# Kernel optimization log

Hardware: AMD Instinct MI355X
Metric: run time of the kernel (lower is better)

Reference implementation:

```python
import jax, jax.numpy as jnp
import numpy as np

B, N, M, C, H = 2, 2048, 512, 1536, 12
HD = C // H          # 128 head dim
RD = 64              # partial rotary dim (rotary_dim in torch code)
EPS = 1e-6


def setup_inputs() -> dict:
    key = jax.random.key(0)
    ks = jax.random.split(key, 8)
    x = jax.random.normal(ks[0], (B, N, C), dtype=jnp.float32)
    y = jax.random.normal(ks[1], (B, M, C), dtype=jnp.float32)
    # realistic rope table: pos[n, j, 0]=cos, pos[n, j, 1]=sin, j over RD//2 freqs
    t = jnp.arange(N, dtype=jnp.float32)
    inv_freq = 1.0 / (10000.0 ** (jnp.arange(RD // 2, dtype=jnp.float32) / (RD // 2)))
    ang = t[:, None] * inv_freq[None, :]                     # [N, RD/2]
    pos = jnp.stack([jnp.cos(ang), jnp.sin(ang)], axis=-1)   # [N, RD/2, 2]
    y_token_weights = jax.random.uniform(ks[2], (B, M), dtype=jnp.float32, minval=0.05, maxval=2.0)
    s = 0.02
    Wqkv = jax.random.normal(ks[3], (C, 3 * C), dtype=jnp.float32) * s
    Wkv = jax.random.normal(ks[4], (C, 2 * C), dtype=jnp.float32) * s
    q_norm_w = jnp.ones((HD,), dtype=jnp.float32)
    k_norm_w = jnp.ones((HD,), dtype=jnp.float32)
    Wproj = jax.random.normal(ks[5], (C, C), dtype=jnp.float32) * s
    bproj = jnp.zeros((C,), dtype=jnp.float32)
    return {"x": x, "y": y, "pos": pos, "y_token_weights": y_token_weights,
            "Wqkv": Wqkv, "Wkv": Wkv, "q_norm_w": q_norm_w, "k_norm_w": k_norm_w,
            "Wproj": Wproj, "bproj": bproj}


def _rms_norm(h, w):
    # RMSNorm in fp32 then cast back (matches torch Norm)
    hf = h.astype(jnp.float32)
    var = jnp.mean(hf * hf, axis=-1, keepdims=True)
    return (w * (hf * jax.lax.rsqrt(var + EPS))).astype(h.dtype)


def _rope(q, k, pos):
    # q,k: [B,H,N,HD]; pos: [N, RD/2, 2]; rotate first RD dims only
    cos = pos[..., 0][None, None]            # [1,1,N,RD/2]
    sin = pos[..., 1][None, None]
    half = RD // 2

    def rot(t):
        t1 = t[..., :half]
        t2 = t[..., half:RD]
        t_rot = jnp.concatenate([t1 * cos - t2 * sin, t1 * sin + t2 * cos], axis=-1)
        return jnp.concatenate([t_rot, t[..., RD:]], axis=-1)

    return rot(q), rot(k)


def reference(x, y, pos, y_token_weights, Wqkv, Wkv, q_norm_w, k_norm_w, Wproj, bproj):
    # self QKV: [B,N,3C] -> [3,B,H,N,HD]
    qkv = jnp.einsum('bnc,cd->bnd', x, Wqkv).reshape(B, N, 3, H, HD).transpose(2, 0, 3, 1, 4)
    q, kx, vx = qkv[0], qkv[1], qkv[2]
    q = _rms_norm(q, q_norm_w)
    kx = _rms_norm(kx, k_norm_w)
    q, kx = _rope(q, kx, pos)

    # cross KV from y: [B,M,2C] -> [2,B,H,M,HD]
    kv = jnp.einsum('bmc,cd->bmd', y, Wkv).reshape(B, M, 2, H, HD).transpose(2, 0, 3, 1, 4)
    ky = _rms_norm(kv[0], k_norm_w)
    vy = kv[1]
    k = jnp.concatenate([kx, ky], axis=2)    # [B,H,N+M,HD]
    v = jnp.concatenate([vx, vy], axis=2)

    # additive bias: zeros over x tokens, log(clamp(w)) over y tokens
    y_bias = jnp.log(jnp.clip(y_token_weights, 1e-4, None))           # [B,M]
    attn_bias = jnp.concatenate([jnp.zeros((B, N), x.dtype), y_bias], axis=1)[:, None, None, :]

    scale = HD ** -0.5
    scores = jnp.einsum('bhnd,bhsd->bhns', q, k) * scale + attn_bias  # [B,H,N,N+M]
    attn = jax.nn.softmax(scores, axis=-1)
    out = jnp.einsum('bhns,bhsd->bhnd', attn, v)                      # [B,H,N,HD]
    out = out.transpose(0, 2, 1, 3).reshape(B, N, C)
    return jnp.einsum('bnc,cd->bnd', out, Wproj) + bproj
```

## Files before the change

kernel.cpp:

```cpp
#include <hip/hip_runtime.h>

typedef unsigned short u16;
typedef short bf16x8 __attribute__((ext_vector_type(8)));
typedef float f32x4 __attribute__((ext_vector_type(4)));
typedef u16 u16x4 __attribute__((ext_vector_type(4)));

#define DEVFN static __device__ __forceinline__

constexpr int Bz = 2, Nn = 2048, Mm = 512, Cc = 1536, Hh = 12, HD = 128;
constexpr int Ss = Nn + Mm;
constexpr float EPSV = 1e-6f;
constexpr float SCL = 0.08838834764831845f;

DEVFN u16 f2bf(float f) {
  union { float f; unsigned u; } v; v.f = f;
  unsigned r = v.u + 0x7fffu + ((v.u >> 16) & 1u);
  return (u16)(r >> 16);
}

DEVFN unsigned cvtpk(float lo, float hi) {
  unsigned r;
  asm("v_cvt_pk_bf16_f32 %0, %1, %2" : "=v"(r) : "v"(lo), "v"(hi));
  return r;
}

DEVFN void gload16(const void* g, void* l) {
  __builtin_amdgcn_global_load_lds((const __attribute__((address_space(1))) void*)g,
                                   (__attribute__((address_space(3))) void*)l, 16, 0, 0);
}

DEVFN f32x4 mfma16(bf16x8 a, bf16x8 b, f32x4 c) {
  return __builtin_amdgcn_mfma_f32_16x16x32_bf16(a, b, c, 0, 0, 0);
}


__global__ void k_convert(const float* __restrict__ in, u16* __restrict__ out, int n) {
  int i = (blockIdx.x * blockDim.x + threadIdx.x) * 4;
  if (i < n) {
    float4 v = *(const float4*)(in + i);
    u16x4 o = { f2bf(v.x), f2bf(v.y), f2bf(v.z), f2bf(v.w) };
    *(u16x4*)(out + i) = o;
  }
}

__global__ void k_transpose_conv(const float* __restrict__ in, u16* __restrict__ out,
                                 int R, int Ccols) {
  __shared__ float t[32][33];
  int c0 = blockIdx.x * 32, r0 = blockIdx.y * 32;
  int lr = threadIdx.x >> 5, lc = threadIdx.x & 31;
#pragma unroll
  for (int i = 0; i < 4; ++i)
    t[lr + 8 * i][lc] = in[(long)(r0 + lr + 8 * i) * Ccols + c0 + lc];
  __syncthreads();
#pragma unroll
  for (int i = 0; i < 4; ++i)
    out[(long)(c0 + lr + 8 * i) * R + r0 + lc] = f2bf(t[lc][lr + 8 * i]);
}

__global__ void k_transpose_v(const u16* __restrict__ in, u16* __restrict__ out) {
  __shared__ u16 t[32][33];
  int bh = blockIdx.z;
  const u16* ib = in + (long)bh * Ss * HD;
  u16* ob = out + (long)bh * HD * Ss;
  int s0 = blockIdx.x * 32, d0 = blockIdx.y * 32;
  int lr = threadIdx.x >> 5, lc = threadIdx.x & 31;
#pragma unroll
  for (int i = 0; i < 4; ++i)
    t[lr + 8 * i][lc] = ib[(long)(s0 + lr + 8 * i) * HD + d0 + lc];
  __syncthreads();
#pragma unroll
  for (int i = 0; i < 4; ++i)
    ob[(long)(d0 + lr + 8 * i) * Ss + s0 + lc] = t[lc][lr + 8 * i];
}

__global__ void k_bias(const float* __restrict__ w, float* __restrict__ bias) {
  int i = blockIdx.x * 256 + threadIdx.x;
  if (i < Bz * Ss) {
    int b = i / Ss, s = i % Ss;
    bias[i] = (s < Nn) ? 0.0f : logf(fmaxf(w[b * Mm + s - Nn], 1e-4f));
  }
}

template <int MODE>
__global__ __launch_bounds__(256, 2) void k_gemm(
    const u16* __restrict__ A, const u16* __restrict__ Bt,
    int K, int NC, int rowsPerB,
    const float* __restrict__ pos, const float* __restrict__ qnw,
    const float* __restrict__ knw, const float* __restrict__ bprj,
    u16* __restrict__ qout, u16* __restrict__ kout, u16* __restrict__ vout,
    float* __restrict__ fout) {
  __shared__ __align__(16) u16 As[128 * 32];
  __shared__ __align__(16) u16 Bs[128 * 32];
  __shared__ float red[256];
  const int tid = threadIdx.x;
  const int lane = tid & 63;
  const int wid = tid >> 6;
  const int g = lane >> 4, cl = lane & 15;
  const int wr = wid >> 1, wc = wid & 1;
  const long m0 = (long)blockIdx.x * 128, n0 = (long)blockIdx.y * 128;

  f32x4 acc[4][4] = {};

  const int trA = tid >> 2;
  const int db = (tid & 3) ^ (trA & 3);
  const char* Ab = (const char*)A + (m0 + trA) * (long)K * 2 + db * 16;
  const char* Bb = (const char*)Bt + (n0 + trA) * (long)K * 2 + db * 16;
  const long rstep = (long)64 * K * 2;
  char* dstA0 = (char*)As + ((tid & ~63) << 4);
  char* dstB0 = (char*)Bs + ((tid & ~63) << 4);

  for (int kt = 0; kt < K / 32; ++kt) {
    __syncthreads();
    gload16(Ab + kt * 64, dstA0);
    gload16(Ab + kt * 64 + rstep, dstA0 + 4096);
    gload16(Bb + kt * 64, dstB0);
    gload16(Bb + kt * 64 + rstep, dstB0 + 4096);
    __syncthreads();
    bf16x8 af[4], bfr[4];
#pragma unroll
    for (int m = 0; m < 4; ++m) {
      int row = wr * 64 + m * 16 + cl;
      af[m] = *(const bf16x8*)((const char*)As + row * 64 + ((g ^ (row & 3)) << 4));
    }
#pragma unroll
    for (int n = 0; n < 4; ++n) {
      int row = wc * 64 + n * 16 + cl;
      bfr[n] = *(const bf16x8*)((const char*)Bs + row * 64 + ((g ^ (row & 3)) << 4));
    }
#pragma unroll
    for (int m = 0; m < 4; ++m)
#pragma unroll
      for (int n = 0; n < 4; ++n)
        acc[m][n] = mfma16(af[m], bfr[n], acc[m][n]);
  }

  if (MODE == 0) {
#pragma unroll
    for (int n = 0; n < 4; ++n) {
      int col = (int)n0 + wc * 64 + n * 16 + cl;
      float bv = bprj[col];
#pragma unroll
      for (int m = 0; m < 4; ++m)
#pragma unroll
        for (int r = 0; r < 4; ++r) {
          long row = m0 + wr * 64 + m * 16 + 4 * g + r;
          fout[row * NC + col] = acc[m][n][r] + bv;
        }
    }
    return;
  }

  const int ct = blockIdx.y;
  const int s_idx = ct / Hh, h = ct % Hh;
  const int bb = (int)(m0 / rowsPerB);
  const int bh = bb * Hh + h;
  const int seq0 = (int)(m0 % rowsPerB) + wr * 64;
  const bool do_norm = (MODE == 1) ? (s_idx < 2) : (s_idx == 0);
  const bool do_rope = (MODE == 1) && (s_idx < 2);

  if (do_norm) {
    float rs[4][4];
#pragma unroll
    for (int m = 0; m < 4; ++m)
#pragma unroll
      for (int r = 0; r < 4; ++r) {
        float t = 0.f;
#pragma unroll
        for (int n = 0; n < 4; ++n) t += acc[m][n][r] * acc[m][n][r];
        t += __shfl_xor(t, 1);
        t += __shfl_xor(t, 2);
        t += __shfl_xor(t, 4);
        t += __shfl_xor(t, 8);
        if (cl == 0) red[wc * 128 + wr * 64 + m * 16 + 4 * g + r] = t;
      }
    __syncthreads();
#pragma unroll
    for (int m = 0; m < 4; ++m)
#pragma unroll
      for (int r = 0; r < 4; ++r) {
        int row = wr * 64 + m * 16 + 4 * g + r;
        rs[m][r] = rsqrtf((red[row] + red[128 + row]) * (1.0f / 128.0f) + EPSV);
      }
    const float* nw = (MODE == 1 && s_idx == 0) ? qnw : knw;
    const float nsc = (MODE == 1 && s_idx == 0) ? SCL : 1.0f;
#pragma unroll
    for (int n = 0; n < 4; ++n) {
      float nwv = nw[wc * 64 + n * 16 + cl] * nsc;
#pragma unroll
      for (int m = 0; m < 4; ++m)
#pragma unroll
        for (int r = 0; r < 4; ++r) acc[m][n][r] *= rs[m][r] * nwv;
    }
  }

  if (do_rope && wc == 0) {
#pragma unroll
    for (int m = 0; m < 4; ++m)
#pragma unroll
      for (int r = 0; r < 4; ++r) {
        int seq = seq0 + m * 16 + 4 * g + r;
#pragma unroll
        for (int n = 0; n < 2; ++n) {
          int d = n * 16 + cl;
          float cs = pos[(seq * 32 + d) * 2 + 0];
          float sn = pos[(seq * 32 + d) * 2 + 1];
          float t1 = acc[m][n][r], t2 = acc[m][n + 2][r];
          acc[m][n][r] = t1 * cs - t2 * sn;
          acc[m][n + 2][r] = t1 * sn + t2 * cs;
        }
      }
  }

  u16* ob;
  long sbase;
  if (MODE == 1) {
    if (s_idx == 0) { ob = qout; sbase = (long)bh * Nn; }
    else if (s_idx == 1) { ob = kout; sbase = (long)bh * Ss; }
    else { ob = vout; sbase = (long)bh * Ss; }
  } else {
    ob = (s_idx == 0) ? kout : vout;
    sbase = (long)bh * Ss + Nn;
  }
#pragma unroll
  for (int m = 0; m < 4; ++m)
#pragma unroll
    for (int r = 0; r < 4; ++r) {
      long rowb = (sbase + seq0 + m * 16 + 4 * g + r) * HD;
#pragma unroll
      for (int n = 0; n < 4; ++n)
        ob[rowb + wc * 64 + n * 16 + cl] = f2bf(acc[m][n][r]);
    }
}

__global__ __launch_bounds__(256, 2) void k_flash(
    const u16* __restrict__ Q, const u16* __restrict__ K, const u16* __restrict__ Vt,
    const float* __restrict__ bias, u16* __restrict__ Aout) {
  __shared__ __align__(16) u16 Ks[2][64 * 128];
  __shared__ __align__(16) u16 Vs[2][128 * 64];
  __shared__ __align__(16) u16 Ps[4][16 * 64];
  const int tid = threadIdx.x, lane = tid & 63, wid = tid >> 6;
  const int g = lane >> 4, cl = lane & 15;
  const int bh = blockIdx.y, b = bh / Hh, h = bh % Hh;
  const int n0 = blockIdx.x * 128;
  constexpr int NT = Ss / 64;

  const u16* Qg = Q + ((long)bh * Nn + n0 + wid * 32) * HD;
  const char* Kg = (const char*)(K + (long)bh * Ss * HD);
  const char* Vg = (const char*)(Vt + (long)bh * HD * Ss);
  const float* bg = bias + b * Ss;

  bf16x8 qf[2][4];
#pragma unroll
  for (int m = 0; m < 2; ++m)
#pragma unroll
    for (int kk = 0; kk < 4; ++kk)
      qf[m][kk] = *(const bf16x8*)(Qg + (m * 16 + cl) * HD + kk * 32 + g * 8);

  const int krow = tid >> 4;
  const char* Ksrc = Kg + krow * 256 + (((tid & 15) ^ (krow & 7)) << 4);
  const int vrow = tid >> 3;
  const char* Vsrc = Vg + (long)vrow * (Ss * 2) + (((tid & 7) ^ (vrow & 7)) << 4);
  const int dsto = (tid & ~63) << 4;

  auto STAGE = [&](int t, int s) {
    char* kd = (char*)Ks[s] + dsto;
    char* vd = (char*)Vs[s] + dsto;
    long kb = (long)t * 64;
#pragma unroll
    for (int i = 0; i < 4; ++i) gload16(Ksrc + kb * 256 + i * (16 * 256), kd + i * 4096);
#pragma unroll
    for (int i = 0; i < 4; ++i) gload16(Vsrc + kb * 2 + (long)i * 32 * (Ss * 2), vd + i * 4096);
  };

  f32x4 ov[2][8] = {};
  float mi[2] = {-3e38f, -3e38f}, li[2] = {0.f, 0.f};
  u16* pt = (u16*)Ps[wid];
  const int h7 = (cl & 7) << 1;

  STAGE(0, 0);
  __syncthreads();
  int cur = 0;
  for (int t = 0; t < NT; ++t) {
    if (t + 1 < NT) STAGE(t + 1, cur ^ 1);
    const bool biased = (t * 64 >= Nn);
    float badd[4][4];
    if (biased) {
#pragma unroll
      for (int n = 0; n < 4; ++n)
#pragma unroll
        for (int r = 0; r < 4; ++r)
          badd[n][r] = bg[t * 64 + n * 16 + 4 * g + r];
    }
    const char* ks = (const char*)Ks[cur];
    const char* vs = (const char*)Vs[cur];

    f32x4 sc[2][4] = {};
#pragma unroll
    for (int n = 0; n < 4; ++n) {
      int krw = n * 16 + cl;
#pragma unroll
      for (int kk = 0; kk < 4; ++kk) {
        bf16x8 kf = *(const bf16x8*)(ks + krw * 256 + (((kk * 4 + g) ^ (krw & 7)) << 4));
        sc[0][n] = mfma16(kf, qf[0][kk], sc[0][n]);
        sc[1][n] = mfma16(kf, qf[1][kk], sc[1][n]);
      }
    }

    float co_s[2];
#pragma unroll
    for (int m = 0; m < 2; ++m) {
      float mx = -3e38f;
#pragma unroll
      for (int n = 0; n < 4; ++n)
#pragma unroll
        for (int r = 0; r < 4; ++r) {
          float s = sc[m][n][r];
          if (biased) s += badd[n][r];
          sc[m][n][r] = s;
          mx = fmaxf(mx, s);
        }
      mx = fmaxf(mx, __shfl_xor(mx, 16));
      mx = fmaxf(mx, __shfl_xor(mx, 32));
      float mnew = fmaxf(mi[m], mx);
      float co = __expf(mi[m] - mnew);
      mi[m] = mnew;
      float rsum = 0.f;
#pragma unroll
      for (int n = 0; n < 4; ++n)
#pragma unroll
        for (int r = 0; r < 4; ++r) {
          float p = __expf(sc[m][n][r] - mnew);
          sc[m][n][r] = p;
          rsum += p;
        }
      rsum += __shfl_xor(rsum, 16);
      rsum += __shfl_xor(rsum, 32);
      li[m] = li[m] * co + rsum;
      co_s[m] = co;
    }

#pragma unroll
    for (int m = 0; m < 2; ++m)
#pragma unroll
      for (int r = 0; r < 4; ++r) {
        float cr = __shfl(co_s[m], 4 * g + r, 64);
#pragma unroll
        for (int nd = 0; nd < 8; ++nd) ov[m][nd][r] *= cr;
      }

    bf16x8 pf[2][2];
#pragma unroll
    for (int m = 0; m < 2; ++m) {
#pragma unroll
      for (int n = 0; n < 4; ++n) {
        uint2 w;
        w.x = cvtpk(sc[m][n][0], sc[m][n][1]);
        w.y = cvtpk(sc[m][n][2], sc[m][n][3]);
        *(uint2*)((char*)pt + cl * 128 + (((4 * n + g) ^ h7) << 3)) = w;
      }
#pragma unroll
      for (int ks2 = 0; ks2 < 2; ++ks2)
        pf[m][ks2] = *(const bf16x8*)((const char*)pt + cl * 128 +
                                      (((8 * ks2 + 2 * g) ^ h7) << 3));
    }

#pragma unroll
    for (int nd = 0; nd < 8; ++nd) {
      int vrw = nd * 16 + cl;
#pragma unroll
      for (int ks2 = 0; ks2 < 2; ++ks2) {
        bf16x8 vf = *(const bf16x8*)(vs + vrw * 128 + (((ks2 * 4 + g) ^ (vrw & 7)) << 4));
        ov[0][nd] = mfma16(pf[0][ks2], vf, ov[0][nd]);
        ov[1][nd] = mfma16(pf[1][ks2], vf, ov[1][nd]);
      }
    }
    __syncthreads();
    cur ^= 1;
  }

#pragma unroll
  for (int m = 0; m < 2; ++m) {
    float inv = 1.0f / li[m];
#pragma unroll
    for (int r = 0; r < 4; ++r) {
      float iv = __shfl(inv, 4 * g + r, 64);
      long row = (long)b * Nn + n0 + wid * 32 + m * 16 + 4 * g + r;
      long base = row * Cc + h * HD;
#pragma unroll
      for (int nd = 0; nd < 8; ++nd)
        Aout[base + nd * 16 + cl] = f2bf(ov[m][nd][r] * iv);
    }
  }
}


extern "C" void kernel_launch(void* const* d_in, const int* in_sizes, int n_in,
                              void* d_out, int out_size, void* d_ws, size_t ws_size,
                              hipStream_t stream) {
  const float* x = (const float*)d_in[0];
  const float* y = (const float*)d_in[1];
  const float* pos = (const float*)d_in[2];
  const float* ytw = (const float*)d_in[3];
  const float* Wqkv = (const float*)d_in[4];
  const float* Wkv = (const float*)d_in[5];
  const float* qnw = (const float*)d_in[6];
  const float* knw = (const float*)d_in[7];
  const float* Wproj = (const float*)d_in[8];
  const float* bproj = (const float*)d_in[9];
  float* out = (float*)d_out;
  char* ws = (char*)d_ws;

  size_t o = 0;
  auto take = [&](size_t b) {
    char* p = ws + o;
    o += (b + 255) & ~(size_t)255;
    return p;
  };
  u16* xb = (u16*)take((size_t)Bz * Nn * Cc * 2);
  u16* yb = (u16*)take((size_t)Bz * Mm * Cc * 2);
  u16* wqkvt = (u16*)take((size_t)3 * Cc * Cc * 2);
  u16* wkvt = (u16*)take((size_t)2 * Cc * Cc * 2);
  u16* wprjt = (u16*)take((size_t)Cc * Cc * 2);
  u16* qb = (u16*)take((size_t)Bz * Hh * Nn * HD * 2);
  u16* kb = (u16*)take((size_t)Bz * Hh * Ss * HD * 2);
  u16* vb = (u16*)take((size_t)Bz * Hh * Ss * HD * 2);
  u16* vtb = (u16*)take((size_t)Bz * Hh * Ss * HD * 2);
  u16* ab = (u16*)take((size_t)Bz * Nn * Cc * 2);
  float* bias = (float*)take((size_t)Bz * Ss * 4);

  k_convert<<<dim3(Bz * Nn * Cc / 1024), 256, 0, stream>>>(x, xb, Bz * Nn * Cc);
  k_convert<<<dim3(Bz * Mm * Cc / 1024), 256, 0, stream>>>(y, yb, Bz * Mm * Cc);
  k_transpose_conv<<<dim3(3 * Cc / 32, Cc / 32), 256, 0, stream>>>(Wqkv, wqkvt, Cc, 3 * Cc);
  k_transpose_conv<<<dim3(2 * Cc / 32, Cc / 32), 256, 0, stream>>>(Wkv, wkvt, Cc, 2 * Cc);
  k_transpose_conv<<<dim3(Cc / 32, Cc / 32), 256, 0, stream>>>(Wproj, wprjt, Cc, Cc);
  k_bias<<<dim3((Bz * Ss + 255) / 256), 256, 0, stream>>>(ytw, bias);
  k_gemm<1><<<dim3(Bz * Nn / 128, 3 * Cc / 128), 256, 0, stream>>>(
      xb, wqkvt, Cc, 3 * Cc, Nn, pos, qnw, knw, nullptr, qb, kb, vb, nullptr);
  k_gemm<2><<<dim3(Bz * Mm / 128, 2 * Cc / 128), 256, 0, stream>>>(
      yb, wkvt, Cc, 2 * Cc, Mm, pos, qnw, knw, nullptr, nullptr, kb, vb, nullptr);
  k_transpose_v<<<dim3(Ss / 32, HD / 32, Bz * Hh), 256, 0, stream>>>(vb, vtb);
  k_flash<<<dim3(Nn / 128, Bz * Hh), 256, 0, stream>>>(qb, kb, vtb, bias, ab);
  k_gemm<0><<<dim3(Bz * Nn / 128, Cc / 128), 256, 0, stream>>>(
      ab, wprjt, Cc, Cc, Nn, nullptr, nullptr, nullptr, bproj, nullptr, nullptr, nullptr, out);
}
```

Baseline: 427.4 us.

## Double-buffer GEMM K-loop with 64-wide tiles and write V transposed from epilogue

The GEMM main loop now uses 64-wide K tiles in two shared-memory buffers, loading the next tile while MFMAs consume the current one. That halves the barriers per K step and hides global-load latency. The QKV and KV GEMM epilogues also write V directly in the transposed [bh, d, s] layout, which removes the separate transpose kernel and its intermediate buffer. The costs are a larger LDS footprint (about 64KB per block), which may limit the 2-blocks-per-CU occupancy target, and strided 8-byte stores for V.

```diff
diff --git a/kernel.cpp b/kernel.cpp
--- a/kernel.cpp
+++ b/kernel.cpp
@@ -55,22 +55,6 @@
 #pragma unroll
   for (int i = 0; i < 4; ++i)
     out[(long)(c0 + lr + 8 * i) * R + r0 + lc] = f2bf(t[lc][lr + 8 * i]);
-}
-
-__global__ void k_transpose_v(const u16* __restrict__ in, u16* __restrict__ out) {
-  __shared__ u16 t[32][33];
-  int bh = blockIdx.z;
-  const u16* ib = in + (long)bh * Ss * HD;
-  u16* ob = out + (long)bh * HD * Ss;
-  int s0 = blockIdx.x * 32, d0 = blockIdx.y * 32;
-  int lr = threadIdx.x >> 5, lc = threadIdx.x & 31;
-#pragma unroll
-  for (int i = 0; i < 4; ++i)
-    t[lr + 8 * i][lc] = ib[(long)(s0 + lr + 8 * i) * HD + d0 + lc];
-  __syncthreads();
-#pragma unroll
-  for (int i = 0; i < 4; ++i)
-    ob[(long)(d0 + lr + 8 * i) * Ss + s0 + lc] = t[lc][lr + 8 * i];
 }
 
 __global__ void k_bias(const float* __restrict__ w, float* __restrict__ bias) {
@@ -89,8 +73,8 @@
     const float* __restrict__ knw, const float* __restrict__ bprj,
     u16* __restrict__ qout, u16* __restrict__ kout, u16* __restrict__ vout,
     float* __restrict__ fout) {
-  __shared__ __align__(16) u16 As[128 * 32];
-  __shared__ __align__(16) u16 Bs[128 * 32];
+  __shared__ __align__(16) u16 As[2][128 * 64];
+  __shared__ __align__(16) u16 Bs[2][128 * 64];
   __shared__ float red[256];
   const int tid = threadIdx.x;
   const int lane = tid & 63;
@@ -101,37 +85,52 @@
 
   f32x4 acc[4][4] = {};
 
-  const int trA = tid >> 2;
-  const int db = (tid & 3) ^ (trA & 3);
-  const char* Ab = (const char*)A + (m0 + trA) * (long)K * 2 + db * 16;
-  const char* Bb = (const char*)Bt + (n0 + trA) * (long)K * 2 + db * 16;
-  const long rstep = (long)64 * K * 2;
-  char* dstA0 = (char*)As + ((tid & ~63) << 4);
-  char* dstB0 = (char*)Bs + ((tid & ~63) << 4);
-
-  for (int kt = 0; kt < K / 32; ++kt) {
+  const int arow0 = tid >> 3;
+  const int sxb = (((tid & 7) ^ (arow0 & 7)) << 4);
+  const long K2 = (long)K * 2;
+  const char* Abase = (const char*)A + (m0 + arow0) * K2 + sxb;
+  const char* Bbase = (const char*)Bt + (n0 + arow0) * K2 + sxb;
+  const int dtid = tid * 16;
+
+  auto STAGE = [&](int kt, int s) {
+    char* ad = (char*)As[s];
+    char* bd = (char*)Bs[s];
+    const long ko = (long)kt * 128;
+#pragma unroll
+    for (int i = 0; i < 4; ++i) {
+      gload16(Abase + i * 32 * K2 + ko, ad + i * 4096 + dtid);
+      gload16(Bbase + i * 32 * K2 + ko, bd + i * 4096 + dtid);
+    }
+  };
+
+  const int nt = K / 64;
+  STAGE(0, 0);
+  int cur = 0;
+  for (int kt = 0; kt < nt; ++kt) {
     __syncthreads();
-    gload16(Ab + kt * 64, dstA0);
-    gload16(Ab + kt * 64 + rstep, dstA0 + 4096);
-    gload16(Bb + kt * 64, dstB0);
-    gload16(Bb + kt * 64 + rstep, dstB0 + 4096);
-    __syncthreads();
-    bf16x8 af[4], bfr[4];
-#pragma unroll
-    for (int m = 0; m < 4; ++m) {
-      int row = wr * 64 + m * 16 + cl;
-      af[m] = *(const bf16x8*)((const char*)As + row * 64 + ((g ^ (row & 3)) << 4));
-    }
-#pragma unroll
-    for (int n = 0; n < 4; ++n) {
-      int row = wc * 64 + n * 16 + cl;
-      bfr[n] = *(const bf16x8*)((const char*)Bs + row * 64 + ((g ^ (row & 3)) << 4));
-    }
-#pragma unroll
-    for (int m = 0; m < 4; ++m)
-#pragma unroll
-      for (int n = 0; n < 4; ++n)
-        acc[m][n] = mfma16(af[m], bfr[n], acc[m][n]);
+    if (kt + 1 < nt) STAGE(kt + 1, cur ^ 1);
+    const char* as = (const char*)As[cur];
+    const char* bs = (const char*)Bs[cur];
+#pragma unroll
+    for (int s = 0; s < 2; ++s) {
+      bf16x8 af[4], bfr[4];
+#pragma unroll
+      for (int m = 0; m < 4; ++m) {
+        int row = wr * 64 + m * 16 + cl;
+        af[m] = *(const bf16x8*)(as + row * 128 + (((s * 4 + g) ^ (row & 7)) << 4));
+      }
+#pragma unroll
+      for (int n = 0; n < 4; ++n) {
+        int row = wc * 64 + n * 16 + cl;
+        bfr[n] = *(const bf16x8*)(bs + row * 128 + (((s * 4 + g) ^ (row & 7)) << 4));
+      }
+#pragma unroll
+      for (int m = 0; m < 4; ++m)
+#pragma unroll
+        for (int n = 0; n < 4; ++n)
+          acc[m][n] = mfma16(af[m], bfr[n], acc[m][n]);
+    }
+    cur ^= 1;
   }
 
   if (MODE == 0) {
@@ -155,8 +154,25 @@
   const int bb = (int)(m0 / rowsPerB);
   const int bh = bb * Hh + h;
   const int seq0 = (int)(m0 % rowsPerB) + wr * 64;
-  const bool do_norm = (MODE == 1) ? (s_idx < 2) : (s_idx == 0);
+  const bool is_v = (MODE == 1) ? (s_idx == 2) : (s_idx == 1);
+  const bool do_norm = !is_v;
   const bool do_rope = (MODE == 1) && (s_idx < 2);
+
+  if (is_v) {
+    const long s0 = (MODE == 2 ? Nn : 0) + seq0;
+#pragma unroll
+    for (int m = 0; m < 4; ++m) {
+      long sb = s0 + m * 16 + 4 * g;
+#pragma unroll
+      for (int n = 0; n < 4; ++n) {
+        int d = wc * 64 + n * 16 + cl;
+        u16x4 pk = { f2bf(acc[m][n][0]), f2bf(acc[m][n][1]),
+                     f2bf(acc[m][n][2]), f2bf(acc[m][n][3]) };
+        *(u16x4*)(vout + ((long)bh * HD + d) * Ss + sb) = pk;
+      }
+    }
+    return;
+  }
 
   if (do_norm) {
     float rs[4][4];
@@ -215,10 +231,9 @@
   long sbase;
   if (MODE == 1) {
     if (s_idx == 0) { ob = qout; sbase = (long)bh * Nn; }
-    else if (s_idx == 1) { ob = kout; sbase = (long)bh * Ss; }
-    else { ob = vout; sbase = (long)bh * Ss; }
+    else { ob = kout; sbase = (long)bh * Ss; }
   } else {
-    ob = (s_idx == 0) ? kout : vout;
+    ob = kout;
     sbase = (long)bh * Ss + Nn;
   }
 #pragma unroll
@@ -423,7 +438,6 @@
   u16* wprjt = (u16*)take((size_t)Cc * Cc * 2);
   u16* qb = (u16*)take((size_t)Bz * Hh * Nn * HD * 2);
   u16* kb = (u16*)take((size_t)Bz * Hh * Ss * HD * 2);
-  u16* vb = (u16*)take((size_t)Bz * Hh * Ss * HD * 2);
   u16* vtb = (u16*)take((size_t)Bz * Hh * Ss * HD * 2);
   u16* ab = (u16*)take((size_t)Bz * Nn * Cc * 2);
   float* bias = (float*)take((size_t)Bz * Ss * 4);
@@ -435,10 +449,9 @@
   k_transpose_conv<<<dim3(Cc / 32, Cc / 32), 256, 0, stream>>>(Wproj, wprjt, Cc, Cc);
   k_bias<<<dim3((Bz * Ss + 255) / 256), 256, 0, stream>>>(ytw, bias);
   k_gemm<1><<<dim3(Bz * Nn / 128, 3 * Cc / 128), 256, 0, stream>>>(
-      xb, wqkvt, Cc, 3 * Cc, Nn, pos, qnw, knw, nullptr, qb, kb, vb, nullptr);
+      xb, wqkvt, Cc, 3 * Cc, Nn, pos, qnw, knw, nullptr, qb, kb, vtb, nullptr);
   k_gemm<2><<<dim3(Bz * Mm / 128, 2 * Cc / 128), 256, 0, stream>>>(
-      yb, wkvt, Cc, 2 * Cc, Mm, pos, qnw, knw, nullptr, nullptr, kb, vb, nullptr);
-  k_transpose_v<<<dim3(Ss / 32, HD / 32, Bz * Hh), 256, 0, stream>>>(vb, vtb);
+      yb, wkvt, Cc, 2 * Cc, Mm, pos, qnw, knw, nullptr, nullptr, kb, vtb, nullptr);
   k_flash<<<dim3(Nn / 128, Bz * Hh), 256, 0, stream>>>(qb, kb, vtb, bias, ab);
   k_gemm<0><<<dim3(Bz * Nn / 128, Cc / 128), 256, 0, stream>>>(
       ab, wprjt, Cc, Cc, Nn, nullptr, nullptr, nullptr, bproj, nullptr, nullptr, nullptr, out);
```

Measured after the change: 411.4 us. -3.7%, faster.
